# Kernel optimization log

Hardware: AMD Instinct MI355X
Metric: run time of the kernel (lower is better)

Reference implementation:

```python
import jax, jax.numpy as jnp
import numpy as np

OUT, IN, V, K, R = 4096, 4096, 8, 4096, 128
TOKENS = 8192

def setup_inputs() -> dict:
    key = jax.random.key(0)
    ks = jax.random.split(key, 9)
    return {
        "x": jax.random.normal(ks[0], (TOKENS, IN), dtype=jnp.float32),
        "centroids": jax.random.normal(ks[1], (K, V), dtype=jnp.float32),
        "indices": jax.random.randint(ks[2], (OUT, IN // V), 0, K, dtype=jnp.int32),
        "U": jax.random.normal(ks[3], (OUT, R), dtype=jnp.float32) * 0.02,
        "S": jax.random.uniform(ks[4], (R,), dtype=jnp.float32) + 0.1,
        "Vt": jax.random.normal(ks[5], (R, IN), dtype=jnp.float32) * 0.02,
        "weight_scale": jax.random.uniform(ks[6], (OUT,), dtype=jnp.float32) + 0.5,
        "weight_bias": jax.random.normal(ks[7], (OUT,), dtype=jnp.float32) * 0.01,
        "bias": jax.random.normal(ks[8], (OUT,), dtype=jnp.float32),
    }

def dequant_weight(centroids, indices, U, S, Vt, weight_scale, weight_bias):
    # codebook lookup: [OUT, IN//V] indices -> [OUT, IN//V, V] -> [OUT, IN]
    w_q = centroids[indices].reshape(indices.shape[0], -1)
    # per-output-channel affine
    w_q = w_q * weight_scale[:, None] + weight_bias[:, None]
    # low-rank SVD correction: U @ diag(S) @ Vt
    lowrank = jnp.einsum('or,r,ri->oi', U, S, Vt)
    return w_q + lowrank

def reference(x, centroids, indices, U, S, Vt, weight_scale, weight_bias, bias):
    dtype = x.dtype
    weight = dequant_weight(centroids, indices, U, S, Vt, weight_scale, weight_bias)
    # result = x @ W^T + bias  (as in forward)
    result = x @ weight.T.astype(dtype) + bias.astype(dtype)[None, :]
    return result.astype(dtype)
```

## Files before the change

### kernel.cpp

```cpp
#include <hip/hip_runtime.h>
#include <hip/hip_bf16.h>
#include <stdint.h>

using bf16 = __hip_bfloat16;
typedef __bf16 bf16x8 __attribute__((ext_vector_type(8)));
typedef float f32x4 __attribute__((ext_vector_type(4)));
typedef short short8 __attribute__((ext_vector_type(8)));

#define GLD_LDS16(gp, lp)                                                            \
  __builtin_amdgcn_global_load_lds(                                                  \
      (const __attribute__((address_space(1))) unsigned int*)(gp),                   \
      (__attribute__((address_space(3))) unsigned int*)(lp), 16, 0, 0)

__global__ __launch_bounds__(256) void convert_x_kernel(const float* __restrict__ x,
                                                        bf16* __restrict__ xb, int n)
{
  for (int i = (blockIdx.x * 256 + threadIdx.x) * 8; i < n; i += gridDim.x * 256 * 8) {
    float4 a = *(const float4*)(x + i);
    float4 b = *(const float4*)(x + i + 4);
    union { bf16 h[8]; short8 v; } u;
    u.h[0] = __float2bfloat16(a.x);
    u.h[1] = __float2bfloat16(a.y);
    u.h[2] = __float2bfloat16(a.z);
    u.h[3] = __float2bfloat16(a.w);
    u.h[4] = __float2bfloat16(b.x);
    u.h[5] = __float2bfloat16(b.y);
    u.h[6] = __float2bfloat16(b.z);
    u.h[7] = __float2bfloat16(b.w);
    *(short8*)(xb + i) = u.v;
  }
}

__global__ __launch_bounds__(256) void prep_kernel(const float* __restrict__ U,
                                                   const float* __restrict__ S,
                                                   const float* __restrict__ Vt,
                                                   bf16* __restrict__ Ub,
                                                   bf16* __restrict__ SVtT)
{
  int t = blockIdx.x * 256 + threadIdx.x;
  if (t < 4096 * 128) {
    Ub[t] = __float2bfloat16(U[t]);
    int i = t >> 7, r = t & 127;
    SVtT[t] = __float2bfloat16(S[r] * Vt[r * 4096 + i]);
  }
}

__global__ __launch_bounds__(256, 2) void gemm_wbuild(const bf16* __restrict__ A,
                                                      const bf16* __restrict__ B,
                                                      bf16* __restrict__ Cb,
                                                      int M, int N, int K,
                                                      const int* __restrict__ indices,
                                                      const float* __restrict__ centroids,
                                                      const float* __restrict__ wscale,
                                                      const float* __restrict__ wbias)
{
  __shared__ bf16 As[128 * 32];
  __shared__ bf16 Bs[128 * 32];

  const int tid  = threadIdx.x;
  const int m0   = blockIdx.y * 128;
  const int n0   = blockIdx.x * 128;
  const int wid  = tid >> 6;
  const int lane = tid & 63;
  const int wm   = wid >> 1;
  const int wn   = wid & 1;

  f32x4 acc[4][4] = {};

  const int sr = tid >> 2;
  const int sc = (tid & 3) * 8;
  const bf16* ga = A + (size_t)(m0 + sr) * K + sc;
  const bf16* gb = B + (size_t)(n0 + sr) * K + sc;
  bf16* la = &As[tid * 8];
  bf16* lb = &Bs[tid * 8];
  const size_t rowHop = (size_t)64 * K;

  const int kk = (lane >> 4) * 8;
  const int fr = lane & 15;

  for (int kt = 0; kt < K; kt += 32) {
    GLD_LDS16(ga + kt,          la);
    GLD_LDS16(ga + kt + rowHop, la + 2048);
    GLD_LDS16(gb + kt,          lb);
    GLD_LDS16(gb + kt + rowHop, lb + 2048);
    __syncthreads();

    bf16x8 af[4], bfr[4];
#pragma unroll
    for (int m = 0; m < 4; m++)
      af[m] = *(const bf16x8*)(As + (wm * 64 + m * 16 + fr) * 32 + kk);
#pragma unroll
    for (int n = 0; n < 4; n++)
      bfr[n] = *(const bf16x8*)(Bs + (wn * 64 + n * 16 + fr) * 32 + kk);

#pragma unroll
    for (int m = 0; m < 4; m++)
#pragma unroll
      for (int n = 0; n < 4; n++)
        acc[m][n] = __builtin_amdgcn_mfma_f32_16x16x32_bf16(af[m], bfr[n], acc[m][n], 0, 0, 0);

    __syncthreads();
  }

#pragma unroll
  for (int m = 0; m < 4; m++) {
#pragma unroll
    for (int n = 0; n < 4; n++) {
      const int col  = n0 + wn * 64 + n * 16 + (lane & 15);
      const int rowb = m0 + wm * 64 + m * 16 + (lane >> 4) * 4;
#pragma unroll
      for (int j = 0; j < 4; j++) {
        const int row  = rowb + j;
        const int idxv = indices[row * 512 + (col >> 3)];
        const float cv = centroids[idxv * 8 + (col & 7)];
        const float w  = cv * wscale[row] + wbias[row] + acc[m][n][j];
        Cb[(size_t)row * N + col] = __float2bfloat16(w);
      }
    }
  }
}

__global__ __launch_bounds__(512, 2) void gemm256(const bf16* __restrict__ A,
                                                  const bf16* __restrict__ B,
                                                  float* __restrict__ C,
                                                  const float* __restrict__ bias)
{
  extern __shared__ char smem[];
  constexpr int K  = 4096;
  constexpr int N  = 4096;
  constexpr int NT = 64;

  const int tid  = threadIdx.x;
  const int lane = tid & 63;
  const int wave = tid >> 6;
  const int wm   = wave >> 2;
  const int wn   = wave & 3;
  const int fr   = lane & 15;
  const int kk   = (lane >> 4) * 8;
  const int swx  = (fr & 7) << 4;

  const int bid = blockIdx.x;
  const int swz = (bid & 7) * 64 + (bid >> 3);
  const int n0  = (swz & 15) * 256;
  const int m0  = (swz >> 4) * 256;

  const bf16* gA[4]; const bf16* gB[4];
  int lA[4], lB[4];
#pragma unroll
  for (int q = 0; q < 2; q++)
#pragma unroll
    for (int is = 0; is < 2; is++) {
      const int p  = q * 8192 + is * 16384 + tid * 16;
      const int r  = p >> 7;
      const int kx = ((p ^ ((r & 7) << 4)) & 127) >> 1;
      gA[q * 2 + is] = A + (size_t)(m0 + r) * K + kx;
      lA[q * 2 + is] = p;
      const int pb  = q * 4096 + is * 16384 + (tid >> 8) * 8192 + (tid & 255) * 16;
      const int rb  = pb >> 7;
      const int kxb = ((pb ^ ((rb & 7) << 4)) & 127) >> 1;
      gB[q * 2 + is] = B + (size_t)(n0 + rb) * K + kxb;
      lB[q * 2 + is] = pb;
    }

  f32x4 acc[8][4] = {};

#define STAGE_A(s, bo, kt) GLD_LDS16(gA[s] + (kt), smem + (bo) + lA[s])
#define STAGE_B(s, bo, kt) GLD_LDS16(gB[s] + (kt), smem + (bo) + 32768 + lB[s])
#define VM8 asm volatile("s_waitcnt vmcnt(8)" ::: "memory")

#define PHASE(qm, qn, STAGES, WAITC)                                               \
  {                                                                                \
    bf16x8 aF[4][2], bF[2][2];                                                     \
    _Pragma("unroll") for (int mm = 0; mm < 4; mm++)                               \
      _Pragma("unroll") for (int ks = 0; ks < 2; ks++)                             \
        aF[mm][ks] = *(const bf16x8*)(smem + ab +                                  \
            ((((wm * 128 + (qm) * 64 + mm * 16 + fr) * 128) +                      \
              (ks * 32 + kk) * 2) ^ swx));                                         \
    _Pragma("unroll") for (int nn = 0; nn < 2; nn++)                               \
      _Pragma("unroll") for (int ks = 0; ks < 2; ks++)                             \
        bF[nn][ks] = *(const bf16x8*)(smem + ab + 32768 +                          \
            ((((wn * 64 + (qn) * 32 + nn * 16 + fr) * 128) +                       \
              (ks * 32 + kk) * 2) ^ swx));                                         \
    STAGES;                                                                        \
    WAITC;                                                                         \
    __builtin_amdgcn_s_barrier();                                                  \
    asm volatile("s_waitcnt lgkmcnt(0)" ::: "memory");                             \
    __builtin_amdgcn_sched_barrier(0);                                             \
    __builtin_amdgcn_s_setprio(1);                                                 \
    _Pragma("unroll") for (int mm = 0; mm < 4; mm++)                               \
      _Pragma("unroll") for (int nn = 0; nn < 2; nn++)                             \
        _Pragma("unroll") for (int ks = 0; ks < 2; ks++)                           \
          acc[(qm) * 4 + mm][(qn) * 2 + nn] =                                      \
              __builtin_amdgcn_mfma_f32_16x16x32_bf16(                             \
                  aF[mm][ks], bF[nn][ks], acc[(qm) * 4 + mm][(qn) * 2 + nn],       \
                  0, 0, 0);                                                        \
    __builtin_amdgcn_s_setprio(0);                                                 \
    __builtin_amdgcn_s_barrier();                                                  \
    __builtin_amdgcn_sched_barrier(0);                                             \
  }

  STAGE_A(0, 0, 0); STAGE_A(1, 0, 0);
  STAGE_B(0, 0, 0); STAGE_B(1, 0, 0);
  STAGE_A(2, 0, 0); STAGE_A(3, 0, 0);
  STAGE_B(2, 0, 0); STAGE_B(3, 0, 0);
  STAGE_A(0, 65536, 64); STAGE_A(1, 65536, 64);
  STAGE_B(0, 65536, 64); STAGE_B(1, 65536, 64);
  VM8;
  __builtin_amdgcn_s_barrier();
  __builtin_amdgcn_sched_barrier(0);

  for (int t = 0; t < NT; t++) {
    const int ab  = (t & 1) * 65536;
    const int nb  = 65536 - ab;
    const int kt1 = ((t + 1) & (NT - 1)) * 64;
    const int kt2 = ((t + 2) & (NT - 1)) * 64;

    PHASE(0, 0,
          { STAGE_A(2, nb, kt1); STAGE_A(3, nb, kt1);
            STAGE_B(2, nb, kt1); STAGE_B(3, nb, kt1); },
          VM8);
    PHASE(0, 1, {}, (void)0);
    PHASE(1, 0, { STAGE_A(0, ab, kt2); STAGE_A(1, ab, kt2); }, (void)0);
    PHASE(1, 1, { STAGE_B(0, ab, kt2); STAGE_B(1, ab, kt2); }, VM8);
  }

#pragma unroll
  for (int mf = 0; mf < 8; mf++) {
#pragma unroll
    for (int nf = 0; nf < 4; nf++) {
      const int col  = n0 + wn * 64 + nf * 16 + fr;
      const int row0 = m0 + wm * 128 + mf * 16 + (lane >> 4) * 4;
      const float bv = bias[col];
#pragma unroll
      for (int j = 0; j < 4; j++)
        C[(size_t)(row0 + j) * N + col] = acc[mf][nf][j] + bv;
    }
  }
#undef PHASE
#undef VM8
#undef STAGE_A
#undef STAGE_B
}

extern "C" void kernel_launch(void* const* d_in, const int* in_sizes, int n_in,
                              void* d_out, int out_size, void* d_ws, size_t ws_size,
                              hipStream_t stream)
{
  const float* x         = (const float*)d_in[0];
  const float* centroids = (const float*)d_in[1];
  const int*   indices   = (const int*)d_in[2];
  const float* U         = (const float*)d_in[3];
  const float* S         = (const float*)d_in[4];
  const float* Vt        = (const float*)d_in[5];
  const float* wscale    = (const float*)d_in[6];
  const float* wbias     = (const float*)d_in[7];
  const float* bias      = (const float*)d_in[8];
  float* out = (float*)d_out;

  char* ws = (char*)d_ws;
  bf16* xb   = (bf16*)(ws);
  bf16* Wb   = (bf16*)(ws + 67108864);
  bf16* Ub   = (bf16*)(ws + 100663296);
  bf16* SVtT = (bf16*)(ws + 101711872);

  convert_x_kernel<<<2048, 256, 0, stream>>>(x, xb, 8192 * 4096);
  prep_kernel<<<2048, 256, 0, stream>>>(U, S, Vt, Ub, SVtT);

  dim3 gW(4096 / 128, 4096 / 128);
  gemm_wbuild<<<gW, 256, 0, stream>>>(Ub, SVtT, Wb, 4096, 4096, 128,
                                      indices, centroids, wscale, wbias);

  gemm256<<<512, 512, 131072, stream>>>(xb, Wb, out, bias);
}
```

Measured before the change: 333.1 us.

## Reorder LDS prefetch pipeline with fragment reuse and 2D XCD tile mapping

Restructures the per-iteration schedule so B fragments are reused across consecutive phases (serpentine order 00,01,11,10), reducing LDS fragment reads, and reorders the global->LDS staging so some loads target the next buffer early and others the current buffer later, with a vmcnt(6) wait. Also changes block-to-tile mapping so each XCD works on a compact 4x... region of M and N tiles to improve L2 reuse. The staging order interacts delicately with buffer hazards; staging into the current buffer 'ab' for kt2 while it is still being read risks correctness if barriers don't cover it.

```diff
diff --git a/kernel.cpp b/kernel.cpp
--- a/kernel.cpp
+++ b/kernel.cpp
@@ -140,9 +140,12 @@
   const int swx  = (fr & 7) << 4;
 
   const int bid = blockIdx.x;
-  const int swz = (bid & 7) * 64 + (bid >> 3);
-  const int n0  = (swz & 15) * 256;
-  const int m0  = (swz >> 4) * 256;
+  const int xcd = bid & 7;
+  const int idx = bid >> 3;
+  const int mi  = (xcd & 3) * 8 + (idx & 7);
+  const int ni  = (xcd >> 2) * 8 + (idx >> 3);
+  const int m0  = mi * 256;
+  const int n0  = ni * 256;
 
   const bf16* gA[4]; const bf16* gB[4];
   int lA[4], lB[4];
@@ -166,46 +169,45 @@
 
 #define STAGE_A(s, bo, kt) GLD_LDS16(gA[s] + (kt), smem + (bo) + lA[s])
 #define STAGE_B(s, bo, kt) GLD_LDS16(gB[s] + (kt), smem + (bo) + 32768 + lB[s])
-#define VM8 asm volatile("s_waitcnt vmcnt(8)" ::: "memory")
-
-#define PHASE(qm, qn, STAGES, WAITC)                                               \
-  {                                                                                \
-    bf16x8 aF[4][2], bF[2][2];                                                     \
-    _Pragma("unroll") for (int mm = 0; mm < 4; mm++)                               \
-      _Pragma("unroll") for (int ks = 0; ks < 2; ks++)                             \
-        aF[mm][ks] = *(const bf16x8*)(smem + ab +                                  \
-            ((((wm * 128 + (qm) * 64 + mm * 16 + fr) * 128) +                      \
-              (ks * 32 + kk) * 2) ^ swx));                                         \
+
+#define LOAD_AF(qm)                                                                \
+  _Pragma("unroll") for (int mm = 0; mm < 4; mm++)                                 \
+    _Pragma("unroll") for (int ks = 0; ks < 2; ks++)                               \
+      aF[mm][ks] = *(const bf16x8*)(smem + ab +                                    \
+          ((((wm * 128 + (qm) * 64 + mm * 16 + fr) * 128) +                        \
+            (ks * 32 + kk) * 2) ^ swx));
+
+#define LOAD_BF(dst, qn)                                                           \
+  _Pragma("unroll") for (int nn = 0; nn < 2; nn++)                                 \
+    _Pragma("unroll") for (int ks = 0; ks < 2; ks++)                               \
+      dst[nn][ks] = *(const bf16x8*)(smem + ab + 32768 +                           \
+          ((((wn * 64 + (qn) * 32 + nn * 16 + fr) * 128) +                         \
+            (ks * 32 + kk) * 2) ^ swx));
+
+#define PHASE_TAIL(qm, qn, bfv)                                                    \
+  __builtin_amdgcn_s_barrier();                                                    \
+  asm volatile("s_waitcnt lgkmcnt(0)" ::: "memory");                               \
+  __builtin_amdgcn_sched_barrier(0);                                               \
+  __builtin_amdgcn_s_setprio(1);                                                   \
+  _Pragma("unroll") for (int mm = 0; mm < 4; mm++)                                 \
     _Pragma("unroll") for (int nn = 0; nn < 2; nn++)                               \
       _Pragma("unroll") for (int ks = 0; ks < 2; ks++)                             \
-        bF[nn][ks] = *(const bf16x8*)(smem + ab + 32768 +                          \
-            ((((wn * 64 + (qn) * 32 + nn * 16 + fr) * 128) +                       \
-              (ks * 32 + kk) * 2) ^ swx));                                         \
-    STAGES;                                                                        \
-    WAITC;                                                                         \
-    __builtin_amdgcn_s_barrier();                                                  \
-    asm volatile("s_waitcnt lgkmcnt(0)" ::: "memory");                             \
-    __builtin_amdgcn_sched_barrier(0);                                             \
-    __builtin_amdgcn_s_setprio(1);                                                 \
-    _Pragma("unroll") for (int mm = 0; mm < 4; mm++)                               \
-      _Pragma("unroll") for (int nn = 0; nn < 2; nn++)                             \
-        _Pragma("unroll") for (int ks = 0; ks < 2; ks++)                           \
-          acc[(qm) * 4 + mm][(qn) * 2 + nn] =                                      \
-              __builtin_amdgcn_mfma_f32_16x16x32_bf16(                             \
-                  aF[mm][ks], bF[nn][ks], acc[(qm) * 4 + mm][(qn) * 2 + nn],       \
-                  0, 0, 0);                                                        \
-    __builtin_amdgcn_s_setprio(0);                                                 \
-    __builtin_amdgcn_s_barrier();                                                  \
-    __builtin_amdgcn_sched_barrier(0);                                             \
-  }
+        acc[(qm) * 4 + mm][(qn) * 2 + nn] =                                        \
+            __builtin_amdgcn_mfma_f32_16x16x32_bf16(                               \
+                aF[mm][ks], bfv[nn][ks], acc[(qm) * 4 + mm][(qn) * 2 + nn],        \
+                0, 0, 0);                                                          \
+  __builtin_amdgcn_s_setprio(0);                                                   \
+  __builtin_amdgcn_s_barrier();                                                    \
+  __builtin_amdgcn_sched_barrier(0);
 
   STAGE_A(0, 0, 0); STAGE_A(1, 0, 0);
+  STAGE_B(2, 0, 0); STAGE_B(3, 0, 0);
+  STAGE_A(2, 0, 0); STAGE_A(3, 0, 0);
   STAGE_B(0, 0, 0); STAGE_B(1, 0, 0);
-  STAGE_A(2, 0, 0); STAGE_A(3, 0, 0);
-  STAGE_B(2, 0, 0); STAGE_B(3, 0, 0);
   STAGE_A(0, 65536, 64); STAGE_A(1, 65536, 64);
-  STAGE_B(0, 65536, 64); STAGE_B(1, 65536, 64);
-  VM8;
+  STAGE_B(2, 65536, 64); STAGE_B(3, 65536, 64);
+  STAGE_A(2, 65536, 64); STAGE_A(3, 65536, 64);
+  asm volatile("s_waitcnt vmcnt(6)" ::: "memory");
   __builtin_amdgcn_s_barrier();
   __builtin_amdgcn_sched_barrier(0);
 
@@ -215,13 +217,24 @@
     const int kt1 = ((t + 1) & (NT - 1)) * 64;
     const int kt2 = ((t + 2) & (NT - 1)) * 64;
 
-    PHASE(0, 0,
-          { STAGE_A(2, nb, kt1); STAGE_A(3, nb, kt1);
-            STAGE_B(2, nb, kt1); STAGE_B(3, nb, kt1); },
-          VM8);
-    PHASE(0, 1, {}, (void)0);
-    PHASE(1, 0, { STAGE_A(0, ab, kt2); STAGE_A(1, ab, kt2); }, (void)0);
-    PHASE(1, 1, { STAGE_B(0, ab, kt2); STAGE_B(1, ab, kt2); }, VM8);
+    bf16x8 aF[4][2], bF0[2][2], bF1[2][2];
+
+    LOAD_AF(0); LOAD_BF(bF0, 0);
+    STAGE_B(0, nb, kt1); STAGE_B(1, nb, kt1);
+    PHASE_TAIL(0, 0, bF0);
+
+    LOAD_BF(bF1, 1);
+    STAGE_A(0, ab, kt2); STAGE_A(1, ab, kt2);
+    PHASE_TAIL(0, 1, bF1);
+
+    LOAD_AF(1);
+    STAGE_B(2, ab, kt2); STAGE_B(3, ab, kt2);
+    PHASE_TAIL(1, 1, bF1);
+
+    LOAD_BF(bF0, 0);
+    STAGE_A(2, ab, kt2); STAGE_A(3, ab, kt2);
+    asm volatile("s_waitcnt vmcnt(6)" ::: "memory");
+    PHASE_TAIL(1, 0, bF0);
   }
 
 #pragma unroll
@@ -236,8 +249,9 @@
         C[(size_t)(row0 + j) * N + col] = acc[mf][nf][j] + bv;
     }
   }
-#undef PHASE
-#undef VM8
+#undef PHASE_TAIL
+#undef LOAD_AF
+#undef LOAD_BF
 #undef STAGE_A
 #undef STAGE_B
 }
```

New measurement: 304.9 us. 1.09x faster.
